# Kernel optimization log

Hardware: AMD Instinct MI355X
Metric: run time of the kernel (lower is better)

## Reference

```python
import jax, jax.numpy as jnp
import numpy as np
import jax.lax as lax


def _log_bf_np(z, s2, s0):
    # Bayes factor per feature; s0 is the prior precision tau_0[l,k] (scalar)
    s0_inv = 1.0 / s0
    s2ps0inv = s2 + s0_inv
    return 0.5 * (jnp.log(s2) - jnp.log(s2ps0inv) + z ** 2 * (s0_inv / s2ps0inv))


def setup_inputs() -> dict:
    key = jax.random.key(0)
    ks = jax.random.split(key, 8)
    n, p, z, l = 1000, 50000, 20, 10
    data = jax.random.normal(ks[0], (n, p), jnp.float32)
    mean_z = jax.random.normal(ks[1], (n, z), jnp.float32)
    # factor second moment must be PSD with strictly positive diagonal (E_zzk > 0)
    mean_zz = (mean_z.T @ mean_z) / n + jnp.eye(z, dtype=jnp.float32)
    mean_w = jax.random.normal(ks[2], (l, z, p), jnp.float32) * 0.01
    var_w = jax.random.uniform(ks[3], (l, z), jnp.float32, minval=0.1, maxval=1.0)
    alpha = jax.random.uniform(ks[4], (l, z, p), jnp.float32)
    alpha = alpha / jnp.sum(alpha, axis=-1, keepdims=True)
    tau = jnp.asarray(1.5, jnp.float32)
    tau_0 = jax.random.uniform(ks[5], (l, z), jnp.float32, minval=0.5, maxval=2.0)
    pi = jax.random.uniform(ks[6], (z, p), jnp.float32, minval=0.5, maxval=1.5)
    pi = pi / jnp.sum(pi, axis=-1, keepdims=True)
    return {"data": data, "mean_z": mean_z, "mean_zz": mean_zz, "mean_w": mean_w,
            "var_w": var_w, "alpha": alpha, "tau": tau, "tau_0": tau_0, "pi": pi}


def reference(data, mean_z, mean_zz, mean_w, var_w, alpha, tau, tau_0, pi):
    """LoadingModel.update: sequential CAVI over factors (k) and single effects (l).
    mean_w/alpha: [l, z, p]; var_w/tau_0: [l, z]; pi: [z, p]; data: [n, p]; mean_z: [n, z].
    Returns updated (mean_w, var_w, alpha)."""
    l_dim, z_dim, p_dim = mean_w.shape
    # collapsed loading moments: W[k, :] = sum_l mean_w[l,k,:] * alpha[l,k,:]
    W = jnp.sum(mean_w * alpha, axis=0)            # [z, p]
    ZtX = mean_z.T @ data                           # [z, p] (precompute of mean_z[:,k] @ data)
    log_pi = jnp.log(pi)                            # [z, p]

    def factor_step(carry, kdx):
        W, mean_w, var_w, alpha = carry
        E_zzk = mean_zz[kdx, kdx]
        Wk = W[kdx]                                 # [p]
        # Wnk.T @ E_zpzk over j != k  ==  mean_zz[kdx] @ W - E_zzk * Wk (avoids the gather)
        RtZk = ZtX[kdx] - (mean_zz[kdx] @ W - E_zzk * Wk)   # [p]
        log_pi_k = log_pi[kdx]
        s2_s = 1.0 / (E_zzk * tau)
        zs_scale = jnp.sqrt(E_zzk * tau) / E_zzk

        def effect_step(Wk, xs):
            mw_l, a_l, t0_l = xs                    # [p], [p], scalar
            Wkl = Wk - mw_l * a_l                   # remove effect l from residual fit
            E_RtZk = RtZk - E_zzk * Wkl             # [p]
            var_new = jnp.reciprocal(tau * E_zzk + t0_l)   # scalar
            mean_new = tau * var_new * E_RtZk       # [p]
            Z_s = E_RtZk * zs_scale
            log_bf = _log_bf_np(Z_s, s2_s, t0_l)
            alpha_new = jax.nn.softmax(log_pi_k + log_bf)
            Wk_new = Wkl + mean_new * alpha_new
            return Wk_new, (mean_new, var_new, alpha_new)

        Wk_new, (mw_rows, vw_rows, a_rows) = lax.scan(
            effect_step, Wk, (mean_w[:, kdx, :], alpha[:, kdx, :], tau_0[:, kdx]))
        mean_w = mean_w.at[:, kdx, :].set(mw_rows)
        var_w = var_w.at[:, kdx].set(vw_rows)
        alpha = alpha.at[:, kdx, :].set(a_rows)
        W = W.at[kdx].set(Wk_new)
        return (W, mean_w, var_w, alpha), None

    (W, mean_w, var_w, alpha), _ = lax.scan(
        factor_step, (W, mean_w, var_w, alpha), jnp.arange(z_dim))
    return mean_w, var_w, alpha
```

## Files before the change

### kernel.cpp

```cpp
#include <hip/hip_runtime.h>
#include <stdint.h>


#define NTA 128
#define NBLKA 392
#define NT_B 1024
#define NBLK_B 49
#define NWAVE_B (NT_B / 64)
#define PSTRIDE 50176

constexpr int N_DIM = 1000;
constexpr int P_DIM = 50000;
constexpr int Z_DIM = 20;
constexpr int L_DIM = 10;

static_assert(NTA * NBLKA == PSTRIDE, "phase A covers PSTRIDE columns");
static_assert(NT_B * NBLK_B == PSTRIDE, "phase B covers PSTRIDE columns");

using u64 = unsigned long long;

__device__ __forceinline__ float wred_max(float v) {
#pragma unroll
  for (int m = 32; m; m >>= 1) v = fmaxf(v, __shfl_xor(v, m, 64));
  return v;
}
__device__ __forceinline__ float wred_sum(float v) {
#pragma unroll
  for (int m = 32; m; m >>= 1) v += __shfl_xor(v, m, 64);
  return v;
}

__global__ __launch_bounds__(NTA) void precompute_kernel(
    const float* __restrict__ data,
    const float* __restrict__ mean_z,
    const float* __restrict__ mean_zz,
    const float* __restrict__ mean_w_in,
    const float* __restrict__ alpha_in,
    const float* __restrict__ tau_p,
    const float* __restrict__ tau0,
    float* __restrict__ ztx_stash,
    float* __restrict__ W_stash,
    float* __restrict__ out_vw)
{
  const int gid = blockIdx.x * NTA + threadIdx.x;
  const bool active = (gid < P_DIM);

  if (gid < L_DIM * Z_DIM) {
    int k = gid % Z_DIM;
    out_vw[gid] = 1.0f / (tau_p[0] * mean_zz[k * Z_DIM + k] + tau0[gid]);
  }

  float ztx[Z_DIM];
#pragma unroll
  for (int k = 0; k < Z_DIM; k++) ztx[k] = 0.f;
  {
    const float* dcol = data + gid;
#pragma unroll 8
    for (int n = 0; n < N_DIM; n++) {
      float d = active ? dcol[(size_t)n * P_DIM] : 0.f;
#pragma unroll
      for (int k = 0; k < Z_DIM; k++) ztx[k] += mean_z[n * Z_DIM + k] * d;
    }
  }
#pragma unroll
  for (int k = 0; k < Z_DIM; k++) ztx_stash[(size_t)k * PSTRIDE + gid] = ztx[k];

  float W[Z_DIM];
#pragma unroll
  for (int j = 0; j < Z_DIM; j++) W[j] = 0.f;
  for (int l = 0; l < L_DIM; l++) {
#pragma unroll
    for (int j = 0; j < Z_DIM; j++) {
      if (active) {
        size_t idx = ((size_t)(l * Z_DIM + j)) * P_DIM + gid;
        W[j] += mean_w_in[idx] * alpha_in[idx];
      }
    }
  }
#pragma unroll
  for (int j = 0; j < Z_DIM; j++) W_stash[(size_t)j * PSTRIDE + gid] = W[j];
}

__global__ __launch_bounds__(NT_B) void loading_model_seq(
    const float* __restrict__ mean_zz,
    const float* __restrict__ mean_w_in,
    const float* __restrict__ alpha_in,
    const float* __restrict__ tau_p,
    const float* __restrict__ tau0,
    const float* __restrict__ pi,
    const float* __restrict__ ztx_stash,
    const float* __restrict__ W_stash,
    float* __restrict__ out_mw,
    float* __restrict__ out_alpha,
    u64* __restrict__ slots)
{
  const int tid  = threadIdx.x;
  const int blk  = blockIdx.x;
  const int gid  = blk * NT_B + tid;
  const bool active = (gid < P_DIM);
  const int lane = tid & 63;
  const int wid  = tid >> 6;
  const float tau = tau_p[0];

  __shared__ float lds_wmax[NWAVE_B];
  __shared__ float lds_wsum[NWAVE_B];
  __shared__ float lds_lse;

  float ztx[Z_DIM], W[Z_DIM];
#pragma unroll
  for (int k = 0; k < Z_DIM; k++) ztx[k] = ztx_stash[(size_t)k * PSTRIDE + gid];
#pragma unroll
  for (int j = 0; j < Z_DIM; j++) W[j] = W_stash[(size_t)j * PSTRIDE + gid];

  float pival = active ? pi[gid] : 1.0f;
  float mw = 0.f, av = 0.f;
  if (active) { mw = mean_w_in[gid]; av = alpha_in[gid]; }

  const float E0    = mean_zz[0];
  const float ktau0 = tau * E0;
  float cs2   = 1.0f / ktau0;
  float czsc2 = tau / E0;
  float nc0, nc1, nmnc;
  {
    const float t0    = tau0[0];
    const float s0inv = 1.0f / t0;
    const float s2p   = cs2 + s0inv;
    nc0  = 0.5f * (__logf(cs2) - __logf(s2p));
    nc1  = 0.5f * czsc2 * (s0inv / s2p);
    nmnc = tau / (ktau0 + t0);
  }

#pragma unroll
  for (int k = 0; k < Z_DIM; k++) {
    const float E    = mean_zz[k * Z_DIM + k];
    const float ktau = tau * E;

    float acc = 0.f;
#pragma unroll
    for (int j = 0; j < Z_DIM; j++) acc += mean_zz[k * Z_DIM + j] * W[j];
    const float RtZk = ztx[k] - (acc - E * W[k]);
    const float lpk  = active ? __logf(pival) : -INFINITY;
    if (k + 1 < Z_DIM && active) pival = pi[(size_t)(k + 1) * P_DIM + gid];

    float Wk = W[k];
    for (int l = 0; l < L_DIM; l++) {
      const float c0  = nc0;
      const float c1  = nc1;
      const float mnc = nmnc;

      const float Wkl = Wk - mw * av;
      const float E_R = RtZk - E * Wkl;
      const float mean_new = mnc * E_R;
      float logit = lpk + c0 + c1 * E_R * E_R;
      if (!active) logit = -INFINITY;

      const size_t oidx = ((size_t)(l * Z_DIM + k)) * P_DIM + gid;
      if (active) out_mw[oidx] = mean_new;

      float wmax = wred_max(logit);
      float ew   = active ? __expf(logit - wmax) : 0.f;
      float wsum = wred_sum(ew);
      if (lane == 0) { lds_wmax[wid] = wmax; lds_wsum[wid] = wsum; }
      __syncthreads();

      const int s   = k * L_DIM + l + 1;
      const int buf = s & 1;
      if (wid == 0) {
        const int li = lane & (NWAVE_B - 1);
        const bool val = (lane < NWAVE_B);
        float m  = lds_wmax[li];
        float sv = lds_wsum[li];
        m  = val ? m  : -INFINITY;
        sv = val ? sv : 0.f;
        float M = wred_max(m);
        float S = wred_sum(val ? __expf(m - M) * sv : 0.f);
        if (lane == 0) {
          float lse_b = M + __logf(S);
          __hip_atomic_store(&slots[buf * NBLK_B + blk],
                             (((u64)(unsigned)s) << 32) | (u64)__float_as_uint(lse_b),
                             __ATOMIC_RELAXED, __HIP_MEMORY_SCOPE_AGENT);
        }
      }

      float mw_n = 0.f, av_n = 0.f;
      {
        int ln = l + 1, kn = k;
        if (ln == L_DIM) { ln = 0; kn = k + 1; }
        if (kn < Z_DIM) {
          if (active) {
            size_t idx2 = ((size_t)(ln * Z_DIM + kn)) * P_DIM + gid;
            mw_n = mean_w_in[idx2];
            av_n = alpha_in[idx2];
          }
          if (ln == 0) {
            const float En = mean_zz[kn * Z_DIM + kn];
            const float kt = tau * En;
            cs2   = 1.0f / kt;
            czsc2 = tau / En;
          }
          const float t0n   = tau0[ln * Z_DIM + kn];
          const float s0inv = 1.0f / t0n;
          const float s2p   = cs2 + s0inv;
          nc0  = 0.5f * (__logf(cs2) - __logf(s2p));
          nc1  = 0.5f * czsc2 * (s0inv / s2p);
          nmnc = (ln == 0) ? tau / (tau * mean_zz[kn * Z_DIM + kn] + t0n)
                           : tau / (ktau + t0n);
        }
      }

      if (wid == 0) {
        bool need = (lane < NBLK_B);
        u64 raw = 0;
        while (need) {
          raw = __hip_atomic_load(&slots[buf * NBLK_B + lane],
                                  __ATOMIC_RELAXED, __HIP_MEMORY_SCOPE_AGENT);
          if ((unsigned)(raw >> 32) == (unsigned)s) need = false;
        }
        float bl = (lane < NBLK_B) ? __uint_as_float((unsigned)raw) : -INFINITY;
        float M  = wred_max(bl);
        float ps = (lane < NBLK_B) ? __expf(bl - M) : 0.f;
        float S  = wred_sum(ps);
        if (lane == 0) lds_lse = M + __logf(S);
      }
      __syncthreads();

      const float LSEt = lds_lse;
      const float alpha_new = active ? __expf(logit - LSEt) : 0.f;
      Wk = Wkl + mean_new * alpha_new;
      if (active) out_alpha[oidx] = alpha_new;
      mw = mw_n;
      av = av_n;
    }
    W[k] = Wk;
  }
}

extern "C" void kernel_launch(void* const* d_in, const int* in_sizes, int n_in,
                              void* d_out, int out_size, void* d_ws, size_t ws_size,
                              hipStream_t stream) {
  const float* data    = (const float*)d_in[0];
  const float* mean_z  = (const float*)d_in[1];
  const float* mean_zz = (const float*)d_in[2];
  const float* mean_w  = (const float*)d_in[3];
  const float* alpha   = (const float*)d_in[5];
  const float* tau     = (const float*)d_in[6];
  const float* tau0    = (const float*)d_in[7];
  const float* pi      = (const float*)d_in[8];

  float* out_mw    = (float*)d_out;
  float* out_vw    = out_mw + (size_t)L_DIM * Z_DIM * P_DIM;
  float* out_alpha = out_vw + (size_t)L_DIM * Z_DIM;
  u64*   ws        = (u64*)d_ws;

  float* ztx_stash = out_mw;
  float* W_stash   = out_alpha;

  hipMemsetAsync(d_ws, 0, 2 * NBLK_B * sizeof(u64), stream);

  hipLaunchKernelGGL(precompute_kernel, dim3(NBLKA), dim3(NTA), 0, stream,
                     data, mean_z, mean_zz, mean_w, alpha, tau, tau0,
                     ztx_stash, W_stash, out_vw);

  void* args[] = {(void*)&mean_zz, (void*)&mean_w, (void*)&alpha,
                  (void*)&tau, (void*)&tau0, (void*)&pi,
                  (void*)&ztx_stash, (void*)&W_stash,
                  (void*)&out_mw, (void*)&out_alpha, (void*)&ws};
  hipLaunchCooperativeKernel((void*)loading_model_seq, dim3(NBLK_B),
                             dim3(NT_B), args, 0, stream);
}
```

Measured before the change: 1.383 ms.

## Split precompute into partial-sum roles and dedicate wave 0 to grid sync

The precompute kernel now launches nine roles of blocks: four compute partial Z^T X sums over quarters of N, and five compute partial W sums over pairs of L. The partials are stashed separately and summed when the sequential kernel loads them. This spreads the Z^T X reduction over four times more blocks to use more of the GPU. In the sequential cooperative kernel, wave 0 now handles only the cross-block log-sum-exp exchange and polling, while the other 15 waves own 960 columns each and prefetch the next parameters in the meantime. The grid grows to 53 blocks, and the partial stashes add memory traffic and reduction adds.

```diff
diff --git a/kernel.cpp b/kernel.cpp
--- a/kernel.cpp
+++ b/kernel.cpp
@@ -3,19 +3,25 @@
 
 
 #define NTA 128
-#define NBLKA 392
+#define NBA 398
+#define NSZ 4
+#define NSW 5
+#define PSTRIDE 50944
+
 #define NT_B 1024
-#define NBLK_B 49
-#define NWAVE_B (NT_B / 64)
-#define PSTRIDE 50176
+#define NWAVE_B 16
+#define COLS_B 960
+#define NBLK_B 53
 
 constexpr int N_DIM = 1000;
 constexpr int P_DIM = 50000;
 constexpr int Z_DIM = 20;
 constexpr int L_DIM = 10;
 
-static_assert(NTA * NBLKA == PSTRIDE, "phase A covers PSTRIDE columns");
-static_assert(NT_B * NBLK_B == PSTRIDE, "phase B covers PSTRIDE columns");
+static_assert(NTA * NBA == PSTRIDE, "A covers PSTRIDE columns");
+static_assert(NBLK_B * COLS_B >= P_DIM, "B covers all real columns");
+static_assert(NBLK_B * COLS_B <= PSTRIDE, "B stash reads in bounds");
+static_assert(NBLK_B <= 64, "one poll load per lane");
 
 using u64 = unsigned long long;
 
@@ -42,43 +48,57 @@
     float* __restrict__ W_stash,
     float* __restrict__ out_vw)
 {
-  const int gid = blockIdx.x * NTA + threadIdx.x;
-  const bool active = (gid < P_DIM);
-
-  if (gid < L_DIM * Z_DIM) {
-    int k = gid % Z_DIM;
-    out_vw[gid] = 1.0f / (tau_p[0] * mean_zz[k * Z_DIM + k] + tau0[gid]);
-  }
-
-  float ztx[Z_DIM];
-#pragma unroll
-  for (int k = 0; k < Z_DIM; k++) ztx[k] = 0.f;
-  {
-    const float* dcol = data + gid;
+  const int bid  = blockIdx.x;
+  const int role = bid / NBA;
+  const int b2   = bid % NBA;
+  const int col  = b2 * NTA + threadIdx.x;
+  const bool act = (col < P_DIM);
+
+  if (role == 0 && b2 < 2) {
+    int g = b2 * NTA + threadIdx.x;
+    if (g < L_DIM * Z_DIM) {
+      int k = g % Z_DIM;
+      out_vw[g] = 1.0f / (tau_p[0] * mean_zz[k * Z_DIM + k] + tau0[g]);
+    }
+  }
+
+  if (role < NSZ) {
+    const int s  = role;
+    const int n0 = s * (N_DIM / NSZ);
+    const int n1 = n0 + (N_DIM / NSZ);
+    float z[Z_DIM];
+#pragma unroll
+    for (int k = 0; k < Z_DIM; k++) z[k] = 0.f;
+    const float* dcol = data + col;
 #pragma unroll 8
-    for (int n = 0; n < N_DIM; n++) {
-      float d = active ? dcol[(size_t)n * P_DIM] : 0.f;
-#pragma unroll
-      for (int k = 0; k < Z_DIM; k++) ztx[k] += mean_z[n * Z_DIM + k] * d;
-    }
-  }
-#pragma unroll
-  for (int k = 0; k < Z_DIM; k++) ztx_stash[(size_t)k * PSTRIDE + gid] = ztx[k];
-
-  float W[Z_DIM];
-#pragma unroll
-  for (int j = 0; j < Z_DIM; j++) W[j] = 0.f;
-  for (int l = 0; l < L_DIM; l++) {
-#pragma unroll
-    for (int j = 0; j < Z_DIM; j++) {
-      if (active) {
-        size_t idx = ((size_t)(l * Z_DIM + j)) * P_DIM + gid;
-        W[j] += mean_w_in[idx] * alpha_in[idx];
+    for (int n = n0; n < n1; n++) {
+      float d = act ? dcol[(size_t)n * P_DIM] : 0.f;
+#pragma unroll
+      for (int k = 0; k < Z_DIM; k++) z[k] += mean_z[n * Z_DIM + k] * d;
+    }
+#pragma unroll
+    for (int k = 0; k < Z_DIM; k++)
+      ztx_stash[(size_t)(s * Z_DIM + k) * PSTRIDE + col] = z[k];
+  } else {
+    const int s = role - NSZ;
+    float Wp[Z_DIM];
+#pragma unroll
+    for (int j = 0; j < Z_DIM; j++) Wp[j] = 0.f;
+#pragma unroll
+    for (int li = 0; li < 2; li++) {
+      const int l = 2 * s + li;
+#pragma unroll
+      for (int j = 0; j < Z_DIM; j++) {
+        if (act) {
+          size_t idx = ((size_t)(l * Z_DIM + j)) * P_DIM + col;
+          Wp[j] += mean_w_in[idx] * alpha_in[idx];
+        }
       }
     }
-  }
-#pragma unroll
-  for (int j = 0; j < Z_DIM; j++) W_stash[(size_t)j * PSTRIDE + gid] = W[j];
+#pragma unroll
+    for (int j = 0; j < Z_DIM; j++)
+      W_stash[(size_t)(s * Z_DIM + j) * PSTRIDE + col] = Wp[j];
+  }
 }
 
 __global__ __launch_bounds__(NT_B) void loading_model_seq(
@@ -96,10 +116,11 @@
 {
   const int tid  = threadIdx.x;
   const int blk  = blockIdx.x;
-  const int gid  = blk * NT_B + tid;
-  const bool active = (gid < P_DIM);
   const int lane = tid & 63;
   const int wid  = tid >> 6;
+  const bool work = (wid > 0);
+  const int col  = blk * COLS_B + (tid - 64);
+  const bool active = work && (col < P_DIM);
   const float tau = tau_p[0];
 
   __shared__ float lds_wmax[NWAVE_B];
@@ -108,13 +129,25 @@
 
   float ztx[Z_DIM], W[Z_DIM];
 #pragma unroll
-  for (int k = 0; k < Z_DIM; k++) ztx[k] = ztx_stash[(size_t)k * PSTRIDE + gid];
-#pragma unroll
-  for (int j = 0; j < Z_DIM; j++) W[j] = W_stash[(size_t)j * PSTRIDE + gid];
-
-  float pival = active ? pi[gid] : 1.0f;
+  for (int k = 0; k < Z_DIM; k++) ztx[k] = 0.f;
+#pragma unroll
+  for (int j = 0; j < Z_DIM; j++) W[j] = 0.f;
+  if (work) {
+#pragma unroll
+    for (int s = 0; s < NSZ; s++)
+#pragma unroll
+      for (int k = 0; k < Z_DIM; k++)
+        ztx[k] += ztx_stash[(size_t)(s * Z_DIM + k) * PSTRIDE + col];
+#pragma unroll
+    for (int s = 0; s < NSW; s++)
+#pragma unroll
+      for (int j = 0; j < Z_DIM; j++)
+        W[j] += W_stash[(size_t)(s * Z_DIM + j) * PSTRIDE + col];
+  }
+
+  float pival = active ? pi[col] : 1.0f;
   float mw = 0.f, av = 0.f;
-  if (active) { mw = mean_w_in[gid]; av = alpha_in[gid]; }
+  if (active) { mw = mean_w_in[col]; av = alpha_in[col]; }
 
   const float E0    = mean_zz[0];
   const float ktau0 = tau * E0;
@@ -140,7 +173,7 @@
     for (int j = 0; j < Z_DIM; j++) acc += mean_zz[k * Z_DIM + j] * W[j];
     const float RtZk = ztx[k] - (acc - E * W[k]);
     const float lpk  = active ? __logf(pival) : -INFINITY;
-    if (k + 1 < Z_DIM && active) pival = pi[(size_t)(k + 1) * P_DIM + gid];
+    if (k + 1 < Z_DIM && active) pival = pi[(size_t)(k + 1) * P_DIM + col];
 
     float Wk = W[k];
     for (int l = 0; l < L_DIM; l++) {
@@ -154,41 +187,49 @@
       float logit = lpk + c0 + c1 * E_R * E_R;
       if (!active) logit = -INFINITY;
 
-      const size_t oidx = ((size_t)(l * Z_DIM + k)) * P_DIM + gid;
+      const size_t oidx = ((size_t)(l * Z_DIM + k)) * P_DIM + col;
       if (active) out_mw[oidx] = mean_new;
 
       float wmax = wred_max(logit);
       float ew   = active ? __expf(logit - wmax) : 0.f;
       float wsum = wred_sum(ew);
-      if (lane == 0) { lds_wmax[wid] = wmax; lds_wsum[wid] = wsum; }
+      if (work && lane == 0) { lds_wmax[wid] = wmax; lds_wsum[wid] = wsum; }
       __syncthreads();
 
       const int s   = k * L_DIM + l + 1;
       const int buf = s & 1;
+
       if (wid == 0) {
-        const int li = lane & (NWAVE_B - 1);
-        const bool val = (lane < NWAVE_B);
-        float m  = lds_wmax[li];
-        float sv = lds_wsum[li];
-        m  = val ? m  : -INFINITY;
-        sv = val ? sv : 0.f;
-        float M = wred_max(m);
-        float S = wred_sum(val ? __expf(m - M) * sv : 0.f);
+        const bool val = (lane >= 1 && lane < NWAVE_B);
+        float m  = val ? lds_wmax[lane] : -INFINITY;
+        float sv = val ? lds_wsum[lane] : 0.f;
+        float M  = wred_max(m);
+        float S  = wred_sum(val ? __expf(m - M) * sv : 0.f);
         if (lane == 0) {
           float lse_b = M + __logf(S);
           __hip_atomic_store(&slots[buf * NBLK_B + blk],
                              (((u64)(unsigned)s) << 32) | (u64)__float_as_uint(lse_b),
                              __ATOMIC_RELAXED, __HIP_MEMORY_SCOPE_AGENT);
         }
-      }
-
-      float mw_n = 0.f, av_n = 0.f;
-      {
+        bool need = (lane < NBLK_B);
+        u64 raw = 0;
+        while (need) {
+          raw = __hip_atomic_load(&slots[buf * NBLK_B + lane],
+                                  __ATOMIC_RELAXED, __HIP_MEMORY_SCOPE_AGENT);
+          if ((unsigned)(raw >> 32) == (unsigned)s) need = false;
+        }
+        float bl = (lane < NBLK_B) ? __uint_as_float((unsigned)raw) : -INFINITY;
+        float Mg = wred_max(bl);
+        float ps = (lane < NBLK_B) ? __expf(bl - Mg) : 0.f;
+        float Sg = wred_sum(ps);
+        if (lane == 0) lds_lse = Mg + __logf(Sg);
+      } else {
+        float mw_n = 0.f, av_n = 0.f;
         int ln = l + 1, kn = k;
         if (ln == L_DIM) { ln = 0; kn = k + 1; }
         if (kn < Z_DIM) {
           if (active) {
-            size_t idx2 = ((size_t)(ln * Z_DIM + kn)) * P_DIM + gid;
+            size_t idx2 = ((size_t)(ln * Z_DIM + kn)) * P_DIM + col;
             mw_n = mean_w_in[idx2];
             av_n = alpha_in[idx2];
           }
@@ -206,21 +247,8 @@
           nmnc = (ln == 0) ? tau / (tau * mean_zz[kn * Z_DIM + kn] + t0n)
                            : tau / (ktau + t0n);
         }
-      }
-
-      if (wid == 0) {
-        bool need = (lane < NBLK_B);
-        u64 raw = 0;
-        while (need) {
-          raw = __hip_atomic_load(&slots[buf * NBLK_B + lane],
-                                  __ATOMIC_RELAXED, __HIP_MEMORY_SCOPE_AGENT);
-          if ((unsigned)(raw >> 32) == (unsigned)s) need = false;
-        }
-        float bl = (lane < NBLK_B) ? __uint_as_float((unsigned)raw) : -INFINITY;
-        float M  = wred_max(bl);
-        float ps = (lane < NBLK_B) ? __expf(bl - M) : 0.f;
-        float S  = wred_sum(ps);
-        if (lane == 0) lds_lse = M + __logf(S);
+        mw = mw_n;
+        av = av_n;
       }
       __syncthreads();
 
@@ -228,8 +256,6 @@
       const float alpha_new = active ? __expf(logit - LSEt) : 0.f;
       Wk = Wkl + mean_new * alpha_new;
       if (active) out_alpha[oidx] = alpha_new;
-      mw = mw_n;
-      av = av_n;
     }
     W[k] = Wk;
   }
@@ -257,7 +283,8 @@
 
   hipMemsetAsync(d_ws, 0, 2 * NBLK_B * sizeof(u64), stream);
 
-  hipLaunchKernelGGL(precompute_kernel, dim3(NBLKA), dim3(NTA), 0, stream,
+  hipLaunchKernelGGL(precompute_kernel, dim3((NSZ + NSW) * NBA), dim3(NTA),
+                     0, stream,
                      data, mean_z, mean_zz, mean_w, alpha, tau, tau0,
                      ztx_stash, W_stash, out_vw);
 
```

Result: faster. 1.161 ms (-16.1%).
